# Optimization experiments

Hardware: AMD Instinct MI355X
Metric: run time of the kernel (lower is better)

The kernel has to match this reference:

```python
import jax, jax.numpy as jnp
import numpy as np

B, T, IN, H, NCLS = 128, 500, 306, 512, 4


def setup_inputs() -> dict:
    key = jax.random.key(0)
    ks = jax.random.split(key, 12)
    s_in = 1.0 / np.sqrt(H)  # PyTorch RNN init scale: U(-1/sqrt(H), 1/sqrt(H))
    u = lambda k, shape: jax.random.uniform(k, shape, jnp.float32, -s_in, s_in)
    return {
        "x": jax.random.normal(ks[0], (B, T, IN), jnp.float32),
        "W_ih0": u(ks[1], (H, IN)),
        "W_hh0": u(ks[2], (H, H)),
        "b_ih0": u(ks[3], (H,)),
        "b_hh0": u(ks[4], (H,)),
        "W_ih1": u(ks[5], (H, H)),
        "W_hh1": u(ks[6], (H, H)),
        "b_ih1": u(ks[7], (H,)),
        "b_hh1": u(ks[8], (H,)),
        "W_fc": u(ks[9], (NCLS, H)),
        "b_fc": u(ks[10], (NCLS,)),
    }


def _rnn_layer(inp, W_ih, W_hh, b_ih, b_hh):
    # Precompute input contribution for all timesteps: [B, T, H]
    pre = jnp.einsum('bti,hi->bth', inp, W_ih) + b_ih + b_hh
    h0 = jnp.zeros((inp.shape[0], W_hh.shape[0]), inp.dtype)

    def step(h, p_t):  # p_t: [B, H]
        h_new = jnp.tanh(p_t + h @ W_hh.T)
        return h_new, h_new

    _, hs = jax.lax.scan(step, h0, jnp.swapaxes(pre, 0, 1))  # hs: [T, B, H]
    return jnp.swapaxes(hs, 0, 1)  # [B, T, H]


def reference(x, W_ih0, W_hh0, b_ih0, b_hh0, W_ih1, W_hh1, b_ih1, b_hh1, W_fc, b_fc):
    h = _rnn_layer(x, W_ih0, W_hh0, b_ih0, b_hh0)
    h = _rnn_layer(h, W_ih1, W_hh1, b_ih1, b_hh1)
    last = h[:, -1, :]                      # [B, H]
    logits = last @ W_fc.T + b_fc           # [B, NCLS]
    return jax.nn.softmax(logits, axis=1)
```

## Files before the change

### kernel.cpp

```cpp
#include <hip/hip_runtime.h>
#include <cstdint>
#include <cstddef>

#define Bb   128
#define Tt   500
#define INn  306
#define Hh   512
#define GRID 128
#define BH32 (Bb * Hh)

typedef short bf16x8 __attribute__((ext_vector_type(8)));
typedef float f32x4  __attribute__((ext_vector_type(4)));
typedef unsigned short u16t;

union F8 { bf16x8 v; uint4 q; unsigned u[4]; u16t s[8]; };

__device__ __forceinline__ float bf2f(u16t h) {
  unsigned u = ((unsigned)h) << 16;
  return __builtin_bit_cast(float, u);
}
__device__ __forceinline__ u16t f2bf(float f) {
  unsigned u = __builtin_bit_cast(unsigned, f);
  unsigned r = u + 0x7fffu + ((u >> 16) & 1u);
  return (u16t)(r >> 16);
}
__device__ __forceinline__ void splitRNE(float v, u16t& hi, u16t& lo) {
  hi = f2bf(v);
  lo = f2bf(v - bf2f(hi));
}
__device__ __forceinline__ void splitTR(float v, u16t& hi, u16t& lo) {
  unsigned u = __builtin_bit_cast(unsigned, v);
  hi = (u16t)(u >> 16);
  float hf = __builtin_bit_cast(float, u & 0xFFFF0000u);
  lo = (u16t)(__builtin_bit_cast(unsigned, v - hf) >> 16);
}
__device__ __forceinline__ f32x4 MF(const F8& a, const F8& b, f32x4 c) {
  return __builtin_amdgcn_mfma_f32_16x16x32_bf16(a.v, b.v, c, 0, 0, 0);
}

__device__ __forceinline__ void stw(unsigned* p, unsigned v) {
  __hip_atomic_store(p, v, __ATOMIC_RELAXED, __HIP_MEMORY_SCOPE_AGENT);
}
__device__ __forceinline__ void poll(unsigned* p, unsigned v) {
  while (__hip_atomic_load(p, __ATOMIC_RELAXED, __HIP_MEMORY_SCOPE_AGENT) != v)
    __builtin_amdgcn_s_sleep(1);
}


__device__ __forceinline__ void stage_tile(const unsigned* __restrict__ gsrc,
                                           unsigned char* smHi,
                                           unsigned char* smLo, int tid) {
  const int row = tid >> 4;
  const int c0  = tid & 15;
#pragma unroll
  for (int k = 0; k < 8; ++k) {
    const int cg = c0 + k * 16;
    const uint4 w = *(const uint4*)(gsrc + (size_t)row * Hh + (size_t)cg * 4);
    const unsigned hi0 = (w.y & 0xFFFF0000u) | (w.x >> 16);
    const unsigned hi1 = (w.w & 0xFFFF0000u) | (w.z >> 16);
    const unsigned lo0 = (w.y << 16) | (w.x & 0xFFFFu);
    const unsigned lo1 = (w.w << 16) | (w.z & 0xFFFFu);
    const int ch   = cg >> 1;
    const int half = cg & 1;
    const size_t boff = (size_t)row * 1024 + ((size_t)(ch ^ (row & 7)) << 4)
                      + (size_t)half * 8;
    *(uint2*)(smHi + boff) = make_uint2(hi0, hi1);
    *(uint2*)(smLo + boff) = make_uint2(lo0, lo1);
  }
}
__device__ __forceinline__ F8 fragLDS(const unsigned char* smP, int row,
                                      int kc, int quad) {
  const int c = kc * 4 + quad;
  F8 f;
  f.q = *(const uint4*)(smP + (size_t)row * 1024
                        + ((size_t)(c ^ (row & 7)) << 4));
  return f;
}

__global__ __launch_bounds__(256, 1) void rnn_all(
    const float* x,
    const float* Wih0, const float* Whh0, const float* bih0, const float* bhh0,
    const float* Wih1, const float* Whh1, const float* bih1, const float* bhh1,
    const float* Wfc,  const float* bfc,
    float* out, unsigned char* ws)
{
  const int wg   = blockIdx.x;
  const int g    = wg >> 4;
  const int sub  = wg & 15;
  const int tid  = threadIdx.x;
  const int lane = tid & 63;
  const int wave = tid >> 6;
  const int l15  = lane & 15;
  const int quad = lane >> 4;

  __shared__ __align__(16) unsigned char sm[65536];
  unsigned char* smA = sm;
  unsigned char* smB = sm + 16384;
  unsigned char* smC = sm + 32768;
  unsigned char* smD = sm + 49152;

  unsigned* fl = (unsigned*)(ws + (size_t)g * 128);
  unsigned* hb32 = (unsigned*)(ws + 1024);
  unsigned* h0p = hb32;
  unsigned* h1p = hb32 + (size_t)2 * BH32;

  const bool isL0 = (sub < 8);
  const int Mb    = g * 16;
  const int Jb    = (isL0 ? sub : sub - 8) * 64;
  const int jn    = Jb + wave * 16 + l15;
  const int rowA  = Mb + l15;
  const int mOutB = Mb + quad * 4;

  if (isL0) {
    F8 Bxh[10], Bxl[10], Bhh[16], Bhl[16];
#pragma unroll
    for (int kc = 0; kc < 10; ++kc) {
#pragma unroll
      for (int e = 0; e < 8; ++e) {
        const int k = kc * 32 + quad * 8 + e;
        float v = (k < INn) ? Wih0[(size_t)jn * INn + k] : 0.f;
        splitRNE(v, Bxh[kc].s[e], Bxl[kc].s[e]);
      }
    }
#pragma unroll
    for (int kc = 0; kc < 16; ++kc) {
      const float* wr = Whh0 + (size_t)jn * Hh + kc * 32 + quad * 8;
#pragma unroll
      for (int e = 0; e < 8; ++e)
        splitRNE(wr[e], Bhh[kc].s[e], Bhl[kc].s[e]);
    }
    const float bv = bih0[jn] + bhh0[jn];

    for (int t = 0; t < Tt; ++t) {
      F8 xh[10], xl[10];
      {
        const float* xr = x + ((size_t)rowA * Tt + t) * INn;
#pragma unroll
        for (int kc = 0; kc < 10; ++kc) {
          const int kb = kc * 32 + quad * 8;
          float v[8];
          if (kc < 9) {
            const float2* p = (const float2*)(xr + kb);
#pragma unroll
            for (int h2 = 0; h2 < 4; ++h2) {
              float2 w = p[h2];
              v[2 * h2] = w.x; v[2 * h2 + 1] = w.y;
            }
          } else {
#pragma unroll
            for (int e = 0; e < 8; ++e)
              v[e] = (kb + e < INn) ? xr[kb + e] : 0.f;
          }
#pragma unroll
          for (int e = 0; e < 8; ++e) splitTR(v[e], xh[kc].s[e], xl[kc].s[e]);
        }
      }

      if (t >= 1) {
        asm volatile("s_waitcnt vmcnt(0)" ::: "memory");
        __syncthreads();
        if (tid == 0) stw(fl + sub * 2 + ((t - 1) & 1), (unsigned)t);
      }
      if (t >= 1 && tid < 8)
        poll(fl + tid * 2 + ((t - 1) & 1), (unsigned)t);
      if (t >= 2 && tid >= 8 && tid < 16)
        poll(fl + tid * 2 + ((t - 2) & 1), (unsigned)(t - 1));
      __syncthreads();
      asm volatile("buffer_inv sc1" ::: "memory");

      if (t >= 1) {
        stage_tile(h0p + (size_t)((t - 1) & 1) * BH32 + (size_t)Mb * Hh,
                   smA, smB, tid);
        __syncthreads();
      }
      f32x4 ac0 = {bv, bv, bv, bv};
      f32x4 ac1 = {0.f, 0.f, 0.f, 0.f};
      f32x4 ac2 = {0.f, 0.f, 0.f, 0.f};
      if (t >= 1) {
#pragma unroll
        for (int kc = 0; kc < 16; ++kc) {
          F8 ah = fragLDS(smA, l15, kc, quad);
          F8 al = fragLDS(smB, l15, kc, quad);
          ac0 = MF(ah, Bhh[kc], ac0);
          ac1 = MF(ah, Bhl[kc], ac1);
          ac2 = MF(al, Bhh[kc], ac2);
        }
      }
#pragma unroll
      for (int kc = 0; kc < 10; ++kc) {
        ac0 = MF(xh[kc], Bxh[kc], ac0);
        ac1 = MF(xh[kc], Bxl[kc], ac1);
        ac2 = MF(xl[kc], Bxh[kc], ac2);
      }

      unsigned* dst = h0p + (size_t)(t & 1) * BH32;
#pragma unroll
      for (int r = 0; r < 4; ++r) {
        const float v = tanhf(ac0[r] + ac1[r] + ac2[r]);
        u16t hb, lb; splitRNE(v, hb, lb);
        stw(dst + (size_t)(mOutB + r) * Hh + jn,
            ((unsigned)hb << 16) | (unsigned)lb);
      }
    }
    asm volatile("s_waitcnt vmcnt(0)" ::: "memory");
    __syncthreads();
    if (tid == 0) stw(fl + sub * 2 + ((Tt - 1) & 1), (unsigned)Tt);
  } else {
    F8 Bih[16], Bil[16], Bh2[16], Bl2[16];
#pragma unroll
    for (int kc = 0; kc < 16; ++kc) {
      const float* w1 = Wih1 + (size_t)jn * Hh + kc * 32 + quad * 8;
      const float* w2 = Whh1 + (size_t)jn * Hh + kc * 32 + quad * 8;
#pragma unroll
      for (int e = 0; e < 8; ++e) {
        splitRNE(w1[e], Bih[kc].s[e], Bil[kc].s[e]);
        splitRNE(w2[e], Bh2[kc].s[e], Bl2[kc].s[e]);
      }
    }
    const float bv = bih1[jn] + bhh1[jn];

    for (int t = 0; t < Tt; ++t) {
      if (tid < 8)
        poll(fl + tid * 2 + (t & 1), (unsigned)(t + 1));
      if (t >= 1) {
        asm volatile("s_waitcnt vmcnt(0)" ::: "memory");
        __syncthreads();
        if (tid == 0) stw(fl + sub * 2 + ((t - 1) & 1), (unsigned)t);
        if (tid >= 8 && tid < 16)
          poll(fl + tid * 2 + ((t - 1) & 1), (unsigned)t);
      }
      __syncthreads();
      asm volatile("buffer_inv sc1" ::: "memory");

      stage_tile(h0p + (size_t)(t & 1) * BH32 + (size_t)Mb * Hh, smA, smB, tid);
      if (t >= 1)
        stage_tile(h1p + (size_t)((t - 1) & 1) * BH32 + (size_t)Mb * Hh,
                   smC, smD, tid);
      __syncthreads();

      f32x4 ac0 = {bv, bv, bv, bv};
      f32x4 ac1 = {0.f, 0.f, 0.f, 0.f};
      f32x4 ac2 = {0.f, 0.f, 0.f, 0.f};
#pragma unroll
      for (int kc = 0; kc < 16; ++kc) {
        F8 ah = fragLDS(smA, l15, kc, quad);
        F8 al = fragLDS(smB, l15, kc, quad);
        ac0 = MF(ah, Bih[kc], ac0);
        ac1 = MF(ah, Bil[kc], ac1);
        ac2 = MF(al, Bih[kc], ac2);
      }
      if (t >= 1) {
#pragma unroll
        for (int kc = 0; kc < 16; ++kc) {
          F8 ah = fragLDS(smC, l15, kc, quad);
          F8 al = fragLDS(smD, l15, kc, quad);
          ac0 = MF(ah, Bh2[kc], ac0);
          ac1 = MF(ah, Bl2[kc], ac1);
          ac2 = MF(al, Bh2[kc], ac2);
        }
      }

      unsigned* dst = h1p + (size_t)(t & 1) * BH32;
#pragma unroll
      for (int r = 0; r < 4; ++r) {
        const float v = tanhf(ac0[r] + ac1[r] + ac2[r]);
        u16t hb, lb; splitRNE(v, hb, lb);
        stw(dst + (size_t)(mOutB + r) * Hh + jn,
            ((unsigned)hb << 16) | (unsigned)lb);
      }
    }
    asm volatile("s_waitcnt vmcnt(0)" ::: "memory");
    __syncthreads();
    if (tid == 0) stw(fl + sub * 2 + ((Tt - 1) & 1), (unsigned)Tt);

    if (sub == 8) {
      if (tid < 8)
        poll(fl + (8 + tid) * 2 + ((Tt - 1) & 1), (unsigned)Tt);
      __syncthreads();
      asm volatile("buffer_inv sc1" ::: "memory");
      if (tid < 16) {
        const int b = Mb + tid;
        const unsigned* hp = h1p + (size_t)((Tt - 1) & 1) * BH32
                           + (size_t)b * Hh;
        float acc[4] = {bfc[0], bfc[1], bfc[2], bfc[3]};
        for (int j = 0; j < Hh; ++j) {
          const unsigned w = hp[j];
          const float hv = bf2f((u16t)(w >> 16)) + bf2f((u16t)(w & 0xFFFFu));
#pragma unroll
          for (int cc = 0; cc < 4; ++cc) acc[cc] += hv * Wfc[cc * Hh + j];
        }
        const float mx = fmaxf(fmaxf(acc[0], acc[1]), fmaxf(acc[2], acc[3]));
        const float e0 = expf(acc[0] - mx), e1 = expf(acc[1] - mx);
        const float e2 = expf(acc[2] - mx), e3 = expf(acc[3] - mx);
        const float si = 1.f / (e0 + e1 + e2 + e3);
        out[b * 4 + 0] = e0 * si;
        out[b * 4 + 1] = e1 * si;
        out[b * 4 + 2] = e2 * si;
        out[b * 4 + 3] = e3 * si;
      }
    }
  }
}

extern "C" void kernel_launch(void* const* d_in, const int* in_sizes, int n_in,
                              void* d_out, int out_size, void* d_ws, size_t ws_size,
                              hipStream_t stream) {
  const float* x    = (const float*)d_in[0];
  const float* Wih0 = (const float*)d_in[1];
  const float* Whh0 = (const float*)d_in[2];
  const float* bih0 = (const float*)d_in[3];
  const float* bhh0 = (const float*)d_in[4];
  const float* Wih1 = (const float*)d_in[5];
  const float* Whh1 = (const float*)d_in[6];
  const float* bih1 = (const float*)d_in[7];
  const float* bhh1 = (const float*)d_in[8];
  const float* Wfc  = (const float*)d_in[9];
  const float* bfc  = (const float*)d_in[10];
  float* out = (float*)d_out;
  unsigned char* ws = (unsigned char*)d_ws;

  rnn_all<<<dim3(GRID), dim3(256), 0, stream>>>(
      x, Wih0, Whh0, bih0, bhh0, Wih1, Whh1, bih1, bhh1, Wfc, bfc, out, ws);
}
```

Measured before the change: 6.214 ms.

## Remap workgroups so each batch group shares one XCD and use local-cache sync

Changes the block-to-group mapping so the 16 workgroups of one batch group are likely co-scheduled on the same XCD (g = wg & 7). At startup each group checks its hardware XCC IDs, and if all 16 match it runs a templated fast path. That path uses plain volatile stores, L2-scoped buffer_inv and volatile polling instead of agent-scope atomics and sc1 invalidates. The aim is to cut the per-timestep cross-block flag and hidden-state exchange latency by keeping it inside one XCD's L2. It relies on the dispatch order placing a group on a single XCD and falls back to the old path otherwise, at the cost of a handshake and doubled code size.

Measured after the change: 5.150 ms. 1.21x faster.

```diff
diff --git a/kernel.cpp b/kernel.cpp
--- a/kernel.cpp
+++ b/kernel.cpp
@@ -11,6 +11,7 @@
 
 typedef short bf16x8 __attribute__((ext_vector_type(8)));
 typedef float f32x4  __attribute__((ext_vector_type(4)));
+typedef unsigned u32x4 __attribute__((ext_vector_type(4)));
 typedef unsigned short u16t;
 
 union F8 { bf16x8 v; uint4 q; unsigned u[4]; u16t s[8]; };
@@ -41,11 +42,33 @@
 __device__ __forceinline__ void stw(unsigned* p, unsigned v) {
   __hip_atomic_store(p, v, __ATOMIC_RELAXED, __HIP_MEMORY_SCOPE_AGENT);
 }
-__device__ __forceinline__ void poll(unsigned* p, unsigned v) {
-  while (__hip_atomic_load(p, __ATOMIC_RELAXED, __HIP_MEMORY_SCOPE_AGENT) != v)
-    __builtin_amdgcn_s_sleep(1);
-}
-
+__device__ __forceinline__ unsigned ldw(const unsigned* p) {
+  return __hip_atomic_load(p, __ATOMIC_RELAXED, __HIP_MEMORY_SCOPE_AGENT);
+}
+
+
+template<bool FAST>
+__device__ __forceinline__ void stf(unsigned* p, unsigned v) {
+  if constexpr (FAST) *(volatile unsigned*)p = v;
+  else stw(p, v);
+}
+template<bool FAST>
+__device__ __forceinline__ void invL() {
+  if constexpr (FAST) asm volatile("buffer_inv" ::: "memory");
+  else asm volatile("buffer_inv sc1" ::: "memory");
+}
+template<bool FAST>
+__device__ __forceinline__ void fpoll(const unsigned* p, unsigned v) {
+  if constexpr (FAST) {
+    for (;;) {
+      asm volatile("buffer_inv" ::: "memory");
+      if (*(const volatile unsigned*)p == v) break;
+      __builtin_amdgcn_s_sleep(1);
+    }
+  } else {
+    while (ldw(p) != v) __builtin_amdgcn_s_sleep(1);
+  }
+}
 
 __device__ __forceinline__ void stage_tile(const unsigned* __restrict__ gsrc,
                                            unsigned char* smHi,
@@ -55,11 +78,11 @@
 #pragma unroll
   for (int k = 0; k < 8; ++k) {
     const int cg = c0 + k * 16;
-    const uint4 w = *(const uint4*)(gsrc + (size_t)row * Hh + (size_t)cg * 4);
-    const unsigned hi0 = (w.y & 0xFFFF0000u) | (w.x >> 16);
-    const unsigned hi1 = (w.w & 0xFFFF0000u) | (w.z >> 16);
-    const unsigned lo0 = (w.y << 16) | (w.x & 0xFFFFu);
-    const unsigned lo1 = (w.w << 16) | (w.z & 0xFFFFu);
+    const u32x4 w = *(const u32x4*)(gsrc + (size_t)row * Hh + (size_t)cg * 4);
+    const unsigned hi0 = (w[1] & 0xFFFF0000u) | (w[0] >> 16);
+    const unsigned hi1 = (w[3] & 0xFFFF0000u) | (w[2] >> 16);
+    const unsigned lo0 = (w[1] << 16) | (w[0] & 0xFFFFu);
+    const unsigned lo1 = (w[3] << 16) | (w[2] & 0xFFFFu);
     const int ch   = cg >> 1;
     const int half = cg & 1;
     const size_t boff = (size_t)row * 1024 + ((size_t)(ch ^ (row & 7)) << 4)
@@ -77,35 +100,26 @@
   return f;
 }
 
-__global__ __launch_bounds__(256, 1) void rnn_all(
+template<bool FAST>
+__device__ void body(
     const float* x,
     const float* Wih0, const float* Whh0, const float* bih0, const float* bhh0,
     const float* Wih1, const float* Whh1, const float* bih1, const float* bhh1,
-    const float* Wfc,  const float* bfc,
-    float* out, unsigned char* ws)
+    const float* Wfc,  const float* bfc, float* out,
+    unsigned* fl, unsigned* h0p, unsigned* h1p, unsigned char* sm,
+    int sub, int tid, int Mb)
 {
-  const int wg   = blockIdx.x;
-  const int g    = wg >> 4;
-  const int sub  = wg & 15;
-  const int tid  = threadIdx.x;
   const int lane = tid & 63;
   const int wave = tid >> 6;
   const int l15  = lane & 15;
   const int quad = lane >> 4;
 
-  __shared__ __align__(16) unsigned char sm[65536];
   unsigned char* smA = sm;
   unsigned char* smB = sm + 16384;
   unsigned char* smC = sm + 32768;
   unsigned char* smD = sm + 49152;
 
-  unsigned* fl = (unsigned*)(ws + (size_t)g * 128);
-  unsigned* hb32 = (unsigned*)(ws + 1024);
-  unsigned* h0p = hb32;
-  unsigned* h1p = hb32 + (size_t)2 * BH32;
-
   const bool isL0 = (sub < 8);
-  const int Mb    = g * 16;
   const int Jb    = (isL0 ? sub : sub - 8) * 64;
   const int jn    = Jb + wave * 16 + l15;
   const int rowA  = Mb + l15;
@@ -159,14 +173,14 @@
       if (t >= 1) {
         asm volatile("s_waitcnt vmcnt(0)" ::: "memory");
         __syncthreads();
-        if (tid == 0) stw(fl + sub * 2 + ((t - 1) & 1), (unsigned)t);
+        if (tid == 0) stf<FAST>(fl + sub * 2 + ((t - 1) & 1), (unsigned)t);
       }
       if (t >= 1 && tid < 8)
-        poll(fl + tid * 2 + ((t - 1) & 1), (unsigned)t);
+        fpoll<FAST>(fl + tid * 2 + ((t - 1) & 1), (unsigned)t);
       if (t >= 2 && tid >= 8 && tid < 16)
-        poll(fl + tid * 2 + ((t - 2) & 1), (unsigned)(t - 1));
+        fpoll<FAST>(fl + tid * 2 + ((t - 2) & 1), (unsigned)(t - 1));
       __syncthreads();
-      asm volatile("buffer_inv sc1" ::: "memory");
+      invL<FAST>();
 
       if (t >= 1) {
         stage_tile(h0p + (size_t)((t - 1) & 1) * BH32 + (size_t)Mb * Hh,
@@ -198,13 +212,13 @@
       for (int r = 0; r < 4; ++r) {
         const float v = tanhf(ac0[r] + ac1[r] + ac2[r]);
         u16t hb, lb; splitRNE(v, hb, lb);
-        stw(dst + (size_t)(mOutB + r) * Hh + jn,
-            ((unsigned)hb << 16) | (unsigned)lb);
+        stf<FAST>(dst + (size_t)(mOutB + r) * Hh + jn,
+                  ((unsigned)hb << 16) | (unsigned)lb);
       }
     }
     asm volatile("s_waitcnt vmcnt(0)" ::: "memory");
     __syncthreads();
-    if (tid == 0) stw(fl + sub * 2 + ((Tt - 1) & 1), (unsigned)Tt);
+    if (tid == 0) stf<FAST>(fl + sub * 2 + ((Tt - 1) & 1), (unsigned)Tt);
   } else {
     F8 Bih[16], Bil[16], Bh2[16], Bl2[16];
 #pragma unroll
@@ -221,18 +235,19 @@
 
     for (int t = 0; t < Tt; ++t) {
       if (tid < 8)
-        poll(fl + tid * 2 + (t & 1), (unsigned)(t + 1));
+        fpoll<FAST>(fl + tid * 2 + (t & 1), (unsigned)(t + 1));
       if (t >= 1) {
         asm volatile("s_waitcnt vmcnt(0)" ::: "memory");
         __syncthreads();
-        if (tid == 0) stw(fl + sub * 2 + ((t - 1) & 1), (unsigned)t);
+        if (tid == 0) stf<FAST>(fl + sub * 2 + ((t - 1) & 1), (unsigned)t);
         if (tid >= 8 && tid < 16)
-          poll(fl + tid * 2 + ((t - 1) & 1), (unsigned)t);
+          fpoll<FAST>(fl + tid * 2 + ((t - 1) & 1), (unsigned)t);
       }
       __syncthreads();
-      asm volatile("buffer_inv sc1" ::: "memory");
-
-      stage_tile(h0p + (size_t)(t & 1) * BH32 + (size_t)Mb * Hh, smA, smB, tid);
+      invL<FAST>();
+
+      stage_tile(h0p + (size_t)(t & 1) * BH32 + (size_t)Mb * Hh,
+                 smA, smB, tid);
       if (t >= 1)
         stage_tile(h1p + (size_t)((t - 1) & 1) * BH32 + (size_t)Mb * Hh,
                    smC, smD, tid);
@@ -265,26 +280,26 @@
       for (int r = 0; r < 4; ++r) {
         const float v = tanhf(ac0[r] + ac1[r] + ac2[r]);
         u16t hb, lb; splitRNE(v, hb, lb);
-        stw(dst + (size_t)(mOutB + r) * Hh + jn,
-            ((unsigned)hb << 16) | (unsigned)lb);
+        stf<FAST>(dst + (size_t)(mOutB + r) * Hh + jn,
+                  ((unsigned)hb << 16) | (unsigned)lb);
       }
     }
     asm volatile("s_waitcnt vmcnt(0)" ::: "memory");
     __syncthreads();
-    if (tid == 0) stw(fl + sub * 2 + ((Tt - 1) & 1), (unsigned)Tt);
+    if (tid == 0) stf<FAST>(fl + sub * 2 + ((Tt - 1) & 1), (unsigned)Tt);
 
     if (sub == 8) {
       if (tid < 8)
-        poll(fl + (8 + tid) * 2 + ((Tt - 1) & 1), (unsigned)Tt);
+        fpoll<FAST>(fl + (8 + tid) * 2 + ((Tt - 1) & 1), (unsigned)Tt);
       __syncthreads();
-      asm volatile("buffer_inv sc1" ::: "memory");
+      invL<FAST>();
       if (tid < 16) {
         const int b = Mb + tid;
         const unsigned* hp = h1p + (size_t)((Tt - 1) & 1) * BH32
                            + (size_t)b * Hh;
         float acc[4] = {bfc[0], bfc[1], bfc[2], bfc[3]};
         for (int j = 0; j < Hh; ++j) {
-          const unsigned w = hp[j];
+          const unsigned w = *(const volatile unsigned*)(hp + j);
           const float hv = bf2f((u16t)(w >> 16)) + bf2f((u16t)(w & 0xFFFFu));
 #pragma unroll
           for (int cc = 0; cc < 4; ++cc) acc[cc] += hv * Wfc[cc * Hh + j];
@@ -300,6 +315,49 @@
       }
     }
   }
+}
+
+__global__ __launch_bounds__(256, 1) void rnn_all(
+    const float* x,
+    const float* Wih0, const float* Whh0, const float* bih0, const float* bhh0,
+    const float* Wih1, const float* Whh1, const float* bih1, const float* bhh1,
+    const float* Wfc,  const float* bfc,
+    float* out, unsigned char* ws)
+{
+  const int wg  = blockIdx.x;
+  const int g   = wg & 7;
+  const int sub = wg >> 3;
+  const int tid = threadIdx.x;
+
+  __shared__ __align__(16) unsigned char sm[65536];
+
+  unsigned* fl  = (unsigned*)(ws + (size_t)g * 128);
+  unsigned* h0p = (unsigned*)(ws + 1024);
+  unsigned* h1p = h0p + (size_t)2 * BH32;
+  const int Mb  = g * 16;
+
+  unsigned xcc;
+  asm("s_getreg_b32 %0, hwreg(HW_REG_XCC_ID)" : "=s"(xcc));
+  xcc &= 7u;
+  unsigned* xt = h1p + (size_t)1 * BH32 + (size_t)Mb * Hh;
+  if (tid == 0) stw(xt + sub, 0xA5C30000u | xcc);
+  unsigned* xsh = (unsigned*)sm;
+  if (tid < 16) {
+    unsigned v;
+    do { v = ldw(xt + tid); } while ((v & 0xFFFFFFF8u) != 0xA5C30000u);
+    xsh[tid] = v & 7u;
+  }
+  __syncthreads();
+  bool fast = true;
+  for (int i = 0; i < 16; ++i) fast = fast && (xsh[i] == xcc);
+  __syncthreads();
+
+  if (fast)
+    body<true >(x, Wih0, Whh0, bih0, bhh0, Wih1, Whh1, bih1, bhh1,
+                Wfc, bfc, out, fl, h0p, h1p, sm, sub, tid, Mb);
+  else
+    body<false>(x, Wih0, Whh0, bih0, bhh0, Wih1, Whh1, bih1, bhh1,
+                Wfc, bfc, out, fl, h0p, h1p, sm, sub, tid, Mb);
 }
 
 extern "C" void kernel_launch(void* const* d_in, const int* in_sizes, int n_in,
```
